# Performance work log

Hardware: AMD Instinct MI355X
Metric: run time of the kernel (lower is better)

Reference implementation:

```python
import jax, jax.numpy as jnp
import numpy as np

N_NODES = 50000
N_EDGES = 800000
D = 256


def setup_inputs() -> dict:
    key = jax.random.key(0)
    k1, k2, k3 = jax.random.split(key, 3)
    node_features = jax.random.normal(k1, (N_NODES, D), dtype=jnp.float32)
    edge_index = jax.random.randint(k2, (2, N_EDGES), 0, N_NODES, dtype=jnp.int64)
    # GCNConv linear weight (glorot-ish scale) and bias
    W = jax.random.normal(k3, (D, D), dtype=jnp.float32) * (1.0 / np.sqrt(D))
    b = jnp.zeros((D,), dtype=jnp.float32)
    alpha = jnp.full((1,), 0.5, dtype=jnp.float32)
    return {"node_features": node_features, "edge_index": edge_index, "W": W, "b": b, "alpha": alpha}


def _gcn_conv(x, edge_index, W, b):
    # PyG GCNConv: add self-loops, symmetric deg^{-1/2} normalization,
    # x' = W x, out[i] = sum_{j in N(i)} norm_ij * x'_j + b
    N = x.shape[0]
    loop = jnp.arange(N, dtype=edge_index.dtype)
    src = jnp.concatenate([edge_index[0], loop])  # [E+N]
    dst = jnp.concatenate([edge_index[1], loop])
    deg = jax.ops.segment_sum(jnp.ones(src.shape, dtype=x.dtype), dst, num_segments=N)
    dinv = jnp.where(deg > 0, jax.lax.rsqrt(jnp.maximum(deg, 1.0)), 0.0)
    norm = dinv[src] * dinv[dst]  # [E+N]
    h = x @ W.T  # [N, D]
    msg = h[src] * norm[:, None]  # gather + scale
    out = jax.ops.segment_sum(msg, dst, num_segments=N)  # scatter-add to targets
    return out + b


def reference(node_features, edge_index, W, b, alpha):
    updated = _gcn_conv(node_features, edge_index, W, b)
    a = alpha[0]
    # eval mode: dropout = identity; alpha-weighted residual blend
    return a * node_features + (1.0 - a) * updated
```

## Files before the change

### kernel.cpp

```cpp
#include <hip/hip_runtime.h>

#define N_NODES 50000
#define N_EDGES 800000
#define D 256
#define SLOT 64
#define GEMM_BLOCKS 391

typedef unsigned short bf16_t;
typedef __attribute__((ext_vector_type(8))) short short8;
typedef __attribute__((ext_vector_type(8))) unsigned short ushort8_t;
typedef __attribute__((ext_vector_type(4))) float f32x4;

__device__ inline float b2f(bf16_t u) {
    union { float f; unsigned v; } t; t.v = ((unsigned)u) << 16; return t.f;
}
__device__ inline bf16_t f2b(float f) {
    union { float f; unsigned v; } t; t.f = f;
    unsigned u = t.v;
    return (bf16_t)((u + 0x7FFFu + ((u >> 16) & 1u)) >> 16);
}
__device__ inline unsigned cvt_pk_bf16(float lo, float hi) {
    unsigned r;
    asm("v_cvt_pk_bf16_f32 %0, %1, %2" : "=v"(r) : "v"(lo), "v"(hi));
    return r;
}
__device__ inline short8 cvt8(float4 a, float4 b) {
    union { short8 s; unsigned u[4]; } t;
    t.u[0] = cvt_pk_bf16(a.x, a.y);
    t.u[1] = cvt_pk_bf16(a.z, a.w);
    t.u[2] = cvt_pk_bf16(b.x, b.y);
    t.u[3] = cvt_pk_bf16(b.z, b.w);
    return t.s;
}

__global__ void initcur_kernel(int* __restrict__ cursor) {
    int i = blockIdx.x * 256 + threadIdx.x;
    if (i < N_NODES) cursor[i] = i << 6;
}

__global__ __launch_bounds__(512) void k1_kernel(const float* __restrict__ x,
                                                 const float* __restrict__ W,
                                                 bf16_t* __restrict__ h,
                                                 const int* __restrict__ ei,
                                                 int* __restrict__ cursor,
                                                 int* __restrict__ csr_src) {
    __shared__ __align__(16) bf16_t Bs[256 * 256];
    __shared__ __align__(16) bf16_t As[2 * 128 * 32];

    const int tid = threadIdx.x;
    const int row0 = blockIdx.x * 128;

    const int srow = tid >> 2;
    const int sq   = tid & 3;
    int sr = row0 + srow;
    if (sr >= N_NODES) sr = N_NODES - 1;
    const float* agp = &x[(size_t)sr * D + sq * 8];
    float4 areg[16];
#pragma unroll
    for (int s = 0; s < 8; s++) {
        const float4* p = reinterpret_cast<const float4*>(&agp[s * 32]);
        areg[2 * s]     = p[0];
        areg[2 * s + 1] = p[1];
    }

    {
        int e0 = blockIdx.x * 2048 + tid;
        int ss[4], pos[4];
        bool ok[4];
#pragma unroll
        for (int j = 0; j < 4; j++) {
            int e = e0 + j * 512;
            ok[j] = (e < N_EDGES);
            int s = 0, d = 0;
            if (ok[j]) { s = ei[e]; d = ei[N_EDGES + e]; }
            ss[j] = s;
            if (ok[j] && (unsigned)d < (unsigned)N_NODES)
                pos[j] = atomicAdd(&cursor[d], 1);
            else
                ok[j] = false;
        }
#pragma unroll
        for (int j = 0; j < 4; j++)
            if (ok[j]) csr_src[pos[j]] = ss[j];
    }

#pragma unroll
    for (int it = 0; it < 16; it++) {
        int idx = it * 512 + tid;
        int col = idx >> 5;
        int c   = idx & 31;
        const float4* q = reinterpret_cast<const float4*>(&W[(size_t)col * D + c * 8]);
        short8 wv = cvt8(q[0], q[1]);
        int phys = c ^ (col & 7);
        *reinterpret_cast<short8*>(&Bs[col * 256 + (phys << 3)]) = wv;
    }
    __syncthreads();

    const int wid  = tid >> 6;
    const int lane = tid & 63;
    const int wr = wid >> 2;
    const int wc = wid & 3;
    const int lr = lane & 15;
    const int g  = lane >> 4;

    f32x4 acc[4][4] = {};

#pragma unroll
    for (int s = 0; s < 8; s++) {
        *reinterpret_cast<short8*>(
            &As[(s & 1) * 4096 + srow * 32 + ((sq ^ (srow & 3)) << 3)]) =
            cvt8(areg[2 * s], areg[2 * s + 1]);
        __syncthreads();

        short8 a[4], b[4];
#pragma unroll
        for (int m = 0; m < 4; m++) {
            int row = wr * 64 + m * 16 + lr;
            a[m] = *reinterpret_cast<const short8*>(
                &As[(s & 1) * 4096 + row * 32 + ((g ^ (row & 3)) << 3)]);
        }
#pragma unroll
        for (int n = 0; n < 4; n++) {
            int col = wc * 64 + n * 16 + lr;
            int c   = s * 4 + g;
            int phys = c ^ (col & 7);
            b[n] = *reinterpret_cast<const short8*>(&Bs[col * 256 + (phys << 3)]);
        }
#pragma unroll
        for (int m = 0; m < 4; m++)
#pragma unroll
            for (int n = 0; n < 4; n++)
                acc[m][n] = __builtin_amdgcn_mfma_f32_16x16x32_bf16(a[m], b[n], acc[m][n], 0, 0, 0);
    }

#pragma unroll
    for (int m = 0; m < 4; m++) {
        int rbase = row0 + wr * 64 + m * 16 + g * 4;
#pragma unroll
        for (int j = 0; j < 4; j++) {
            int rr = rbase + j;
            if (rr < N_NODES) {
#pragma unroll
                for (int n = 0; n < 4; n++)
                    h[(size_t)rr * D + wc * 64 + n * 16 + lr] = f2b(acc[m][n][j]);
            }
        }
    }
}

__global__ void dinv_kernel(const int* __restrict__ cursor, float* __restrict__ dinv) {
    int i = blockIdx.x * 256 + threadIdx.x;
    if (i < N_NODES) {
        int cnt = cursor[i] - (i << 6);
        dinv[i] = rsqrtf((float)(cnt + 1));
    }
}

__global__ __launch_bounds__(256) void gather_kernel(const int* __restrict__ cursor,
                                                     const int* __restrict__ csr_src,
                                                     const float* __restrict__ dinv,
                                                     const bf16_t* __restrict__ h,
                                                     const float* __restrict__ x,
                                                     const float* __restrict__ b,
                                                     const float* __restrict__ alpha,
                                                     float* __restrict__ out) {
    const int half = (threadIdx.x >> 5) & 1;
    const int wv   = threadIdx.x >> 6;
    const int ln   = threadIdx.x & 31;
    const int n = blockIdx.x * 8 + wv * 2 + half;
    if (n >= N_NODES) return;
    const int col = ln * 8;

    const int beg = n << 6;
    const int end = cursor[n];
    const float dn = dinv[n];
    const bf16_t* hl = h + col;

    float a0 = 0.f, a1 = 0.f, a2 = 0.f, a3 = 0.f,
          a4 = 0.f, a5 = 0.f, a6 = 0.f, a7 = 0.f;
    int k = beg;
    for (; k + 3 < end; k += 4) {
        int s0 = csr_src[k], s1 = csr_src[k + 1], s2 = csr_src[k + 2], s3 = csr_src[k + 3];
        float n0 = dinv[s0] * dn, n1 = dinv[s1] * dn, n2 = dinv[s2] * dn, n3 = dinv[s3] * dn;
        ushort8_t r0 = *reinterpret_cast<const ushort8_t*>(&hl[(size_t)s0 * D]);
        ushort8_t r1 = *reinterpret_cast<const ushort8_t*>(&hl[(size_t)s1 * D]);
        ushort8_t r2 = *reinterpret_cast<const ushort8_t*>(&hl[(size_t)s2 * D]);
        ushort8_t r3 = *reinterpret_cast<const ushort8_t*>(&hl[(size_t)s3 * D]);
        a0 += b2f(r0[0]) * n0 + b2f(r1[0]) * n1 + b2f(r2[0]) * n2 + b2f(r3[0]) * n3;
        a1 += b2f(r0[1]) * n0 + b2f(r1[1]) * n1 + b2f(r2[1]) * n2 + b2f(r3[1]) * n3;
        a2 += b2f(r0[2]) * n0 + b2f(r1[2]) * n1 + b2f(r2[2]) * n2 + b2f(r3[2]) * n3;
        a3 += b2f(r0[3]) * n0 + b2f(r1[3]) * n1 + b2f(r2[3]) * n2 + b2f(r3[3]) * n3;
        a4 += b2f(r0[4]) * n0 + b2f(r1[4]) * n1 + b2f(r2[4]) * n2 + b2f(r3[4]) * n3;
        a5 += b2f(r0[5]) * n0 + b2f(r1[5]) * n1 + b2f(r2[5]) * n2 + b2f(r3[5]) * n3;
        a6 += b2f(r0[6]) * n0 + b2f(r1[6]) * n1 + b2f(r2[6]) * n2 + b2f(r3[6]) * n3;
        a7 += b2f(r0[7]) * n0 + b2f(r1[7]) * n1 + b2f(r2[7]) * n2 + b2f(r3[7]) * n3;
    }
    for (; k < end; k++) {
        int s0 = csr_src[k];
        float n0 = dinv[s0] * dn;
        ushort8_t r0 = *reinterpret_cast<const ushort8_t*>(&hl[(size_t)s0 * D]);
        a0 += b2f(r0[0]) * n0; a1 += b2f(r0[1]) * n0;
        a2 += b2f(r0[2]) * n0; a3 += b2f(r0[3]) * n0;
        a4 += b2f(r0[4]) * n0; a5 += b2f(r0[5]) * n0;
        a6 += b2f(r0[6]) * n0; a7 += b2f(r0[7]) * n0;
    }

    const float dv2 = dn * dn;
    const float a   = alpha[0];
    ushort8_t hv = *reinterpret_cast<const ushort8_t*>(&hl[(size_t)n * D]);
    const float4* xp = reinterpret_cast<const float4*>(&x[(size_t)n * D + col]);
    const float4* bp = reinterpret_cast<const float4*>(&b[col]);
    float4 xv0 = xp[0], xv1 = xp[1];
    float4 bv0 = bp[0], bv1 = bp[1];
    float4 r0, r1;
    r0.x = a * xv0.x + (1.0f - a) * (a0 + dv2 * b2f(hv[0]) + bv0.x);
    r0.y = a * xv0.y + (1.0f - a) * (a1 + dv2 * b2f(hv[1]) + bv0.y);
    r0.z = a * xv0.z + (1.0f - a) * (a2 + dv2 * b2f(hv[2]) + bv0.z);
    r0.w = a * xv0.w + (1.0f - a) * (a3 + dv2 * b2f(hv[3]) + bv0.w);
    r1.x = a * xv1.x + (1.0f - a) * (a4 + dv2 * b2f(hv[4]) + bv1.x);
    r1.y = a * xv1.y + (1.0f - a) * (a5 + dv2 * b2f(hv[5]) + bv1.y);
    r1.z = a * xv1.z + (1.0f - a) * (a6 + dv2 * b2f(hv[6]) + bv1.z);
    r1.w = a * xv1.w + (1.0f - a) * (a7 + dv2 * b2f(hv[7]) + bv1.w);
    float4* op = reinterpret_cast<float4*>(&out[(size_t)n * D + col]);
    op[0] = r0;
    op[1] = r1;
}

extern "C" void kernel_launch(void* const* d_in, const int* in_sizes, int n_in,
                              void* d_out, int out_size, void* d_ws, size_t ws_size,
                              hipStream_t stream) {
    const float* x     = (const float*)d_in[0];
    const int*   ei    = (const int*)d_in[1];
    const float* W     = (const float*)d_in[2];
    const float* b     = (const float*)d_in[3];
    const float* alpha = (const float*)d_in[4];
    float* out = (float*)d_out;

    char* ws = (char*)d_ws;
    const size_t HB = (size_t)N_NODES * D * 2;
    bf16_t* h      = (bf16_t*)ws;
    int*   cursor  = (int*)  (ws + HB);
    float* dinv    = (float*)(ws + HB + 200000);
    int*   csr_src = (int*)  (ws + HB + 400000);

    initcur_kernel<<<(N_NODES + 255) / 256, 256, 0, stream>>>(cursor);
    k1_kernel<<<GEMM_BLOCKS, 512, 0, stream>>>(x, W, h, ei, cursor, csr_src);
    dinv_kernel<<<(N_NODES + 255) / 256, 256, 0, stream>>>(cursor, dinv);
    gather_kernel<<<(N_NODES + 7) / 8, 256, 0, stream>>>(cursor, csr_src, dinv, h, x, b, alpha, out);
}
```

Baseline: 140.9 us.

## Make GEMM+CSR-build kernel persistent over 256 blocks with two tiles each

The fused GEMM and edge-bucketing kernel now launches 256 blocks, one per CU, instead of 391. Each block loops over up to two 128-row tiles, so the bf16 W matrix staged in LDS is loaded once per block rather than once per tile. Each block also bucketizes 4096 edges instead of 2048. The edge loop is simplified to a plain load, atomic, store sequence with no prefetch arrays. The trade-off is that the first A-tile loads no longer overlap with the edge atomics and W staging, and 135 blocks do two tiles while 121 do one, which creates a tail imbalance.

```diff
diff --git a/kernel.cpp b/kernel.cpp
--- a/kernel.cpp
+++ b/kernel.cpp
@@ -4,7 +4,8 @@
 #define N_EDGES 800000
 #define D 256
 #define SLOT 64
-#define GEMM_BLOCKS 391
+#define N_TILES 391
+#define K1_BLOCKS 256
 
 typedef unsigned short bf16_t;
 typedef __attribute__((ext_vector_type(8))) short short8;
@@ -48,40 +49,22 @@
     __shared__ __align__(16) bf16_t As[2 * 128 * 32];
 
     const int tid = threadIdx.x;
-    const int row0 = blockIdx.x * 128;
-
-    const int srow = tid >> 2;
-    const int sq   = tid & 3;
-    int sr = row0 + srow;
-    if (sr >= N_NODES) sr = N_NODES - 1;
-    const float* agp = &x[(size_t)sr * D + sq * 8];
-    float4 areg[16];
-#pragma unroll
-    for (int s = 0; s < 8; s++) {
-        const float4* p = reinterpret_cast<const float4*>(&agp[s * 32]);
-        areg[2 * s]     = p[0];
-        areg[2 * s + 1] = p[1];
-    }
+    const int bid = blockIdx.x;
 
     {
-        int e0 = blockIdx.x * 2048 + tid;
-        int ss[4], pos[4];
-        bool ok[4];
-#pragma unroll
-        for (int j = 0; j < 4; j++) {
+        int e0 = bid * 4096 + tid;
+#pragma unroll
+        for (int j = 0; j < 8; j++) {
             int e = e0 + j * 512;
-            ok[j] = (e < N_EDGES);
-            int s = 0, d = 0;
-            if (ok[j]) { s = ei[e]; d = ei[N_EDGES + e]; }
-            ss[j] = s;
-            if (ok[j] && (unsigned)d < (unsigned)N_NODES)
-                pos[j] = atomicAdd(&cursor[d], 1);
-            else
-                ok[j] = false;
-        }
-#pragma unroll
-        for (int j = 0; j < 4; j++)
-            if (ok[j]) csr_src[pos[j]] = ss[j];
+            if (e < N_EDGES) {
+                int s = ei[e];
+                int d = ei[N_EDGES + e];
+                if ((unsigned)d < (unsigned)N_NODES) {
+                    int pos = atomicAdd(&cursor[d], 1);
+                    csr_src[pos] = s;
+                }
+            }
+        }
     }
 
 #pragma unroll
@@ -102,47 +85,66 @@
     const int wc = wid & 3;
     const int lr = lane & 15;
     const int g  = lane >> 4;
-
-    f32x4 acc[4][4] = {};
-
-#pragma unroll
-    for (int s = 0; s < 8; s++) {
-        *reinterpret_cast<short8*>(
-            &As[(s & 1) * 4096 + srow * 32 + ((sq ^ (srow & 3)) << 3)]) =
-            cvt8(areg[2 * s], areg[2 * s + 1]);
-        __syncthreads();
-
-        short8 a[4], b[4];
+    const int srow = tid >> 2;
+    const int sq   = tid & 3;
+
+    for (int t = 0; t < 2; t++) {
+        const int tile = bid + t * K1_BLOCKS;
+        if (tile >= N_TILES) break;
+        const int row0 = tile * 128;
+
+        int sr = row0 + srow;
+        if (sr >= N_NODES) sr = N_NODES - 1;
+        const float* agp = &x[(size_t)sr * D + sq * 8];
+        float4 areg[16];
+#pragma unroll
+        for (int s = 0; s < 8; s++) {
+            const float4* p = reinterpret_cast<const float4*>(&agp[s * 32]);
+            areg[2 * s]     = p[0];
+            areg[2 * s + 1] = p[1];
+        }
+
+        f32x4 acc[4][4] = {};
+
+#pragma unroll
+        for (int s = 0; s < 8; s++) {
+            *reinterpret_cast<short8*>(
+                &As[(s & 1) * 4096 + srow * 32 + ((sq ^ (srow & 3)) << 3)]) =
+                cvt8(areg[2 * s], areg[2 * s + 1]);
+            __syncthreads();
+
+            short8 a[4], b[4];
+#pragma unroll
+            for (int m = 0; m < 4; m++) {
+                int row = wr * 64 + m * 16 + lr;
+                a[m] = *reinterpret_cast<const short8*>(
+                    &As[(s & 1) * 4096 + row * 32 + ((g ^ (row & 3)) << 3)]);
+            }
+#pragma unroll
+            for (int n = 0; n < 4; n++) {
+                int col = wc * 64 + n * 16 + lr;
+                int c   = s * 4 + g;
+                int phys = c ^ (col & 7);
+                b[n] = *reinterpret_cast<const short8*>(&Bs[col * 256 + (phys << 3)]);
+            }
+#pragma unroll
+            for (int m = 0; m < 4; m++)
+#pragma unroll
+                for (int n = 0; n < 4; n++)
+                    acc[m][n] = __builtin_amdgcn_mfma_f32_16x16x32_bf16(a[m], b[n], acc[m][n], 0, 0, 0);
+        }
+
 #pragma unroll
         for (int m = 0; m < 4; m++) {
-            int row = wr * 64 + m * 16 + lr;
-            a[m] = *reinterpret_cast<const short8*>(
-                &As[(s & 1) * 4096 + row * 32 + ((g ^ (row & 3)) << 3)]);
-        }
-#pragma unroll
-        for (int n = 0; n < 4; n++) {
-            int col = wc * 64 + n * 16 + lr;
-            int c   = s * 4 + g;
-            int phys = c ^ (col & 7);
-            b[n] = *reinterpret_cast<const short8*>(&Bs[col * 256 + (phys << 3)]);
-        }
-#pragma unroll
-        for (int m = 0; m < 4; m++)
-#pragma unroll
-            for (int n = 0; n < 4; n++)
-                acc[m][n] = __builtin_amdgcn_mfma_f32_16x16x32_bf16(a[m], b[n], acc[m][n], 0, 0, 0);
-    }
-
-#pragma unroll
-    for (int m = 0; m < 4; m++) {
-        int rbase = row0 + wr * 64 + m * 16 + g * 4;
-#pragma unroll
-        for (int j = 0; j < 4; j++) {
-            int rr = rbase + j;
-            if (rr < N_NODES) {
-#pragma unroll
-                for (int n = 0; n < 4; n++)
-                    h[(size_t)rr * D + wc * 64 + n * 16 + lr] = f2b(acc[m][n][j]);
+            int rbase = row0 + wr * 64 + m * 16 + g * 4;
+#pragma unroll
+            for (int j = 0; j < 4; j++) {
+                int rr = rbase + j;
+                if (rr < N_NODES) {
+#pragma unroll
+                    for (int n = 0; n < 4; n++)
+                        h[(size_t)rr * D + wc * 64 + n * 16 + lr] = f2b(acc[m][n][j]);
+                }
             }
         }
     }
@@ -244,7 +246,7 @@
     int*   csr_src = (int*)  (ws + HB + 400000);
 
     initcur_kernel<<<(N_NODES + 255) / 256, 256, 0, stream>>>(cursor);
-    k1_kernel<<<GEMM_BLOCKS, 512, 0, stream>>>(x, W, h, ei, cursor, csr_src);
+    k1_kernel<<<K1_BLOCKS, 512, 0, stream>>>(x, W, h, ei, cursor, csr_src);
     dinv_kernel<<<(N_NODES + 255) / 256, 256, 0, stream>>>(cursor, dinv);
     gather_kernel<<<(N_NODES + 7) / 8, 256, 0, stream>>>(cursor, csr_src, dinv, h, x, b, alpha, out);
 }
```

New measurement: 141.2 us. Within noise of the previous version (+0.2%).
